# Optimization experiments

Measured on AMD Instinct MI355X. Metric: run time of the kernel, lower is better.

The kernel has to match this reference:

```python
import jax, jax.numpy as jnp
import numpy as np
from jax import lax

B = 8192
C = 16          # conv_channels
H = 256         # hidden_size = W_init.shape[0]
OUT = 10
IN_SIZE = C * 14 * 14  # 3136


def setup_inputs() -> dict:
    key = jax.random.key(0)
    ks = jax.random.split(key, 8)
    x = jax.random.normal(ks[0], (B, 1, 28, 28), dtype=jnp.float32)
    conv_w = jax.random.normal(ks[1], (C, 1, 3, 3), dtype=jnp.float32) * 0.1
    conv_b = jax.random.normal(ks[2], (C,), dtype=jnp.float32) * 0.1
    W_in = jax.random.normal(ks[3], (H, IN_SIZE), dtype=jnp.float32) * 0.02
    b_in = jax.random.normal(ks[4], (H,), dtype=jnp.float32) * 0.02
    W_out = jax.random.normal(ks[5], (OUT, H), dtype=jnp.float32) * 0.05
    b_out = jax.random.normal(ks[6], (OUT,), dtype=jnp.float32) * 0.05
    # register_buffer('W', W_init * 1e-5)
    W = jax.random.normal(ks[7], (H, H), dtype=jnp.float32) * 1e-5
    return {"x": x, "conv_w": conv_w, "conv_b": conv_b, "W_in": W_in,
            "b_in": b_in, "W_out": W_out, "b_out": b_out, "W": W}


def reference(x, conv_w, conv_b, W_in, b_in, W_out, b_out, W):
    # Conv2d(1, C, 3, padding=1) + ReLU
    y = lax.conv_general_dilated(
        x, conv_w, window_strides=(1, 1), padding="SAME",
        dimension_numbers=("NCHW", "OIHW", "NCHW"))
    y = jax.nn.relu(y + conv_b[None, :, None, None])
    # MaxPool2d(2): 28x28 -> 14x14
    y = lax.reduce_window(y, -jnp.inf, lax.max,
                          (1, 1, 2, 2), (1, 1, 2, 2), "VALID")
    conv_flat = y.reshape(y.shape[0], -1)  # [B, C*14*14], NCHW order matches torch view
    # step 0: E_t = Linear(conv_flat); r_t starts at zeros
    E0 = conv_flat @ W_in.T + b_in            # [B, H]
    r = jax.nn.relu(E0)                       # relu(0 @ W + E0 + 0)
    # 9 more steps with zero input -> E_t = b_in
    for _ in range(9):
        r = jax.nn.relu(r @ W + b_in + r)
    return r @ W_out.T + b_out                # [B, 10]
```

## Files before the change

kernel.cpp:

```cpp
#include <hip/hip_runtime.h>

typedef _Float16 f16x8 __attribute__((ext_vector_type(8)));
typedef _Float16 f16x4 __attribute__((ext_vector_type(4)));
typedef float f32x4 __attribute__((ext_vector_type(4)));

__device__ __forceinline__ void gload16(const void* g, void* l) {
  __builtin_amdgcn_global_load_lds(
      (__attribute__((address_space(1))) void*)g,
      (__attribute__((address_space(3))) void*)l, 16, 0, 0);
}

#define W_SCALE 4096.0f
#define W_UNSCALE (1.0f / 4096.0f)

#define SWZA(k, row) (((k) & ~31) | (((k) & 31) ^ (((row) & 3) << 3)))

__global__ __launch_bounds__(256) void conv_pool_kernel(
    const float* __restrict__ x,
    const float* __restrict__ cw,
    const float* __restrict__ cb,
    _Float16* __restrict__ out) {
  __shared__ float wsm[144];
  __shared__ float bsm[16];
  int tid = threadIdx.x;
  if (tid < 144) wsm[tid] = cw[tid];
  if (tid < 16) bsm[tid] = cb[tid];
  __syncthreads();
  if (tid >= 196) return;
  int b = blockIdx.x;
  int ph = tid / 14, pw = tid - ph * 14;
  const float* xb = x + b * 784;
  float xv[4][4];
  int r0 = 2 * ph - 1, c0 = 2 * pw - 1;
#pragma unroll
  for (int i = 0; i < 4; ++i) {
    int r = r0 + i;
#pragma unroll
    for (int j = 0; j < 4; ++j) {
      int c = c0 + j;
      xv[i][j] = (r >= 0 && r < 28 && c >= 0 && c < 28) ? xb[r * 28 + c] : 0.f;
    }
  }
#pragma unroll
  for (int ch = 0; ch < 16; ++ch) {
    float a0 = bsm[ch], a1 = a0, a2 = a0, a3 = a0;
#pragma unroll
    for (int i = 0; i < 3; ++i)
#pragma unroll
      for (int j = 0; j < 3; ++j) {
        float wv = wsm[ch * 9 + i * 3 + j];
        a0 = fmaf(wv, xv[i][j],     a0);
        a1 = fmaf(wv, xv[i][j + 1], a1);
        a2 = fmaf(wv, xv[i + 1][j],     a2);
        a3 = fmaf(wv, xv[i + 1][j + 1], a3);
      }
    float m = fmaxf(fmaxf(a0, a1), fmaxf(a2, a3));
    m = fmaxf(m, 0.f);
    int k = ch * 196 + tid;
    out[b * 3136 + SWZA(k, b)] = (_Float16)m;
  }
}

__global__ __launch_bounds__(256) void win_cvt_kernel(
    const float* __restrict__ in,
    _Float16* __restrict__ out) {
  int n = blockIdx.x, tid = threadIdx.x;
  const float* src = in + (size_t)n * 3136;
  _Float16* dst = out + (size_t)n * 3136;
#pragma unroll
  for (int it = 0; it < 4; ++it) {
    int idx = it * 256 + tid;
    if (idx < 784) {
      int k0 = idx * 4;
      float4 v = *(const float4*)(src + k0);
      f16x4 h = {(_Float16)v.x, (_Float16)v.y, (_Float16)v.z, (_Float16)v.w};
      *(f16x4*)(dst + SWZA(k0, n)) = h;
    }
  }
}

__global__ void wt_cvt_kernel(const float* __restrict__ W,
                              _Float16* __restrict__ Wt) {
  int i = blockIdx.x * 256 + threadIdx.x;
  int k = i >> 8, n = i & 255;
  Wt[n * 256 + k] = (_Float16)(W[k * 256 + n] * W_SCALE);
}

__global__ __launch_bounds__(256) void gemm1_kernel(
    const _Float16* __restrict__ A,
    const _Float16* __restrict__ Bw,
    const float* __restrict__ bias,
    float* __restrict__ Rf,
    _Float16* __restrict__ Rb) {
  const int K = 3136;
  __shared__ __align__(16) _Float16 As[64 * 32];
  __shared__ __align__(16) _Float16 Bs[128 * 32];
  int tid = threadIdx.x, lane = tid & 63, wid = tid >> 6;
  int bm = blockIdx.x * 64, bn = blockIdx.y * 128;
  f32x4 zero = {0.f, 0.f, 0.f, 0.f};
  f32x4 acc[2][4];
#pragma unroll
  for (int i = 0; i < 2; ++i)
#pragma unroll
    for (int j = 0; j < 4; ++j) acc[i][j] = zero;

  const _Float16* Ag  = A  + (size_t)(bm + wid * 16 + (lane >> 2)) * K + (lane & 3) * 8;
  const _Float16* Bg0 = Bw + (size_t)(bn + wid * 32 + (lane >> 2)) * K + (lane & 3) * 8;
  const _Float16* Bg1 = Bg0 + 16 * K;
  _Float16* Asw  = As + wid * 512;
  _Float16* Bsw0 = Bs + wid * 1024;
  _Float16* Bsw1 = Bsw0 + 512;

  int wm = (wid & 1) * 32, wn = (wid >> 1) * 64;
  int koff = (lane >> 4) * 8;
  for (int k0 = 0; k0 < K; k0 += 32) {
    __syncthreads();
    gload16(Ag + k0, Asw);
    gload16(Bg0 + k0, Bsw0);
    gload16(Bg1 + k0, Bsw1);
    __syncthreads();
    f16x8 af[2];
#pragma unroll
    for (int mi = 0; mi < 2; ++mi) {
      int ar = wm + mi * 16 + (lane & 15);
      af[mi] = *(const f16x8*)(As + ar * 32 + (koff ^ ((ar & 3) << 3)));
    }
#pragma unroll
    for (int ni = 0; ni < 4; ++ni) {
      int br = wn + ni * 16 + (lane & 15);
      f16x8 bf = *(const f16x8*)(Bs + br * 32 + (koff ^ ((br & 3) << 3)));
      acc[0][ni] = __builtin_amdgcn_mfma_f32_16x16x32_f16(af[0], bf, acc[0][ni], 0, 0, 0);
      acc[1][ni] = __builtin_amdgcn_mfma_f32_16x16x32_f16(af[1], bf, acc[1][ni], 0, 0, 0);
    }
  }
  int rg = (lane >> 4) * 4, cl = lane & 15;
#pragma unroll
  for (int mi = 0; mi < 2; ++mi)
#pragma unroll
    for (int ni = 0; ni < 4; ++ni)
#pragma unroll
      for (int j = 0; j < 4; ++j) {
        int m = bm + wm + mi * 16 + rg + j;
        int n = bn + wn + ni * 16 + cl;
        float v = fmaxf(acc[mi][ni][j] + bias[n], 0.f);
        Rf[m * 256 + n] = v;
        Rb[m * 256 + n] = (_Float16)v;
      }
}

__global__ __launch_bounds__(512, 2) void rnn_persist_kernel(
    const _Float16* __restrict__ Rb,
    const float*    __restrict__ Rf,
    const _Float16* __restrict__ Wt,
    const float*    __restrict__ b_in,
    const float*    __restrict__ Wo,
    const float*    __restrict__ bo,
    float*          __restrict__ out)
{
  __shared__ __align__(16) _Float16 r_lds[32 * 256];
  int tid = threadIdx.x, lane = tid & 63, wid = tid >> 6;
  int wr = wid >> 2, wc = wid & 3;
  int bm = blockIdx.x * 32;

  f16x8 wfr[8][4];
#pragma unroll
  for (int kk = 0; kk < 8; ++kk)
#pragma unroll
    for (int ni = 0; ni < 4; ++ni) {
      int n = wc * 64 + ni * 16 + (lane & 15);
      int kpos = kk * 32 + (lane >> 4) * 8;
      wfr[kk][ni] = *(const f16x8*)(Wt + n * 256 + kpos);
    }

  float breg[4];
  float rres[4][4];
  int rrow = wr * 16 + (lane >> 4) * 4;
#pragma unroll
  for (int ni = 0; ni < 4; ++ni) {
    int col = wc * 64 + ni * 16 + (lane & 15);
    breg[ni] = b_in[col];
#pragma unroll
    for (int j = 0; j < 4; ++j)
      rres[ni][j] = Rf[(size_t)(bm + rrow + j) * 256 + col];
  }

#pragma unroll
  for (int it = 0; it < 2; ++it) {
    int idx = it * 512 + tid;
    int row = idx >> 5;
    int kc = (idx & 31) * 8;
    f16x8 v = *(const f16x8*)(Rb + (size_t)(bm + row) * 256 + kc);
    *(f16x8*)(r_lds + row * 256 + (kc ^ ((row & 7) << 3))) = v;
  }

  int arow = wr * 16 + (lane & 15);
  int aswz = (arow & 7) << 3;
  for (int s = 0; s < 9; ++s) {
    __syncthreads();
    f32x4 acc[4];
#pragma unroll
    for (int ni = 0; ni < 4; ++ni) acc[ni] = (f32x4){0.f, 0.f, 0.f, 0.f};
#pragma unroll
    for (int kk = 0; kk < 8; ++kk) {
      int kpos = kk * 32 + (lane >> 4) * 8;
      f16x8 af = *(const f16x8*)(r_lds + arow * 256 + (kpos ^ aswz));
#pragma unroll
      for (int ni = 0; ni < 4; ++ni)
        acc[ni] = __builtin_amdgcn_mfma_f32_16x16x32_f16(af, wfr[kk][ni], acc[ni], 0, 0, 0);
    }
    __syncthreads();
#pragma unroll
    for (int ni = 0; ni < 4; ++ni) {
      int col = wc * 64 + ni * 16 + (lane & 15);
#pragma unroll
      for (int j = 0; j < 4; ++j) {
        float v = fmaxf(fmaf(acc[ni][j], W_UNSCALE, breg[ni] + rres[ni][j]), 0.f);
        rres[ni][j] = v;
        int row = rrow + j;
        r_lds[row * 256 + (col ^ ((row & 7) << 3))] = (_Float16)v;
      }
    }
  }
  __syncthreads();

  if (tid < 320) {
    int row = tid / 10, o = tid - row * 10;
    int rswz = (row & 7) << 3;
    float accd = 0.f;
    for (int kc = 0; kc < 256; kc += 8) {
      f16x8 rv = *(const f16x8*)(r_lds + row * 256 + (kc ^ rswz));
      const float* wp = Wo + o * 256 + kc;
#pragma unroll
      for (int j = 0; j < 8; ++j) accd = fmaf((float)rv[j], wp[j], accd);
    }
    out[(size_t)(bm + row) * 10 + o] = accd + bo[o];
  }
}

extern "C" void kernel_launch(void* const* d_in, const int* in_sizes, int n_in,
                              void* d_out, int out_size, void* d_ws, size_t ws_size,
                              hipStream_t stream) {
  const float* x      = (const float*)d_in[0];
  const float* conv_w = (const float*)d_in[1];
  const float* conv_b = (const float*)d_in[2];
  const float* W_in   = (const float*)d_in[3];
  const float* b_in   = (const float*)d_in[4];
  const float* W_out  = (const float*)d_in[5];
  const float* b_out  = (const float*)d_in[6];
  const float* W      = (const float*)d_in[7];
  float* out = (float*)d_out;

  char* ws = (char*)d_ws;
  size_t o = 0;
  _Float16* conv_flat = (_Float16*)(ws + o); o += (size_t)8192 * 3136 * 2;
  _Float16* W_in_h    = (_Float16*)(ws + o); o += (size_t)256 * 3136 * 2;
  _Float16* Wt_h      = (_Float16*)(ws + o); o += (size_t)256 * 256 * 2;
  float*    Rf0       = (float*)(ws + o);    o += (size_t)8192 * 256 * 4;
  _Float16* Rb0       = (_Float16*)(ws + o); o += (size_t)8192 * 256 * 2;

  win_cvt_kernel<<<256, 256, 0, stream>>>(W_in, W_in_h);
  wt_cvt_kernel<<<256, 256, 0, stream>>>(W, Wt_h);
  conv_pool_kernel<<<8192, 256, 0, stream>>>(x, conv_w, conv_b, conv_flat);
  gemm1_kernel<<<dim3(128, 2), 256, 0, stream>>>(conv_flat, W_in_h, b_in, Rf0, Rb0);
  rnn_persist_kernel<<<256, 512, 0, stream>>>(Rb0, Rf0, Wt_h, b_in, W_out, b_out, out);
}
```

Before: 188.3 us.

## Split-K gemm1 with atomics, interleaved tile layout, packed fp16 conv

Splits the 3136-long K of the first GEMM across 7 z-blocks that accumulate into a bias-initialised fp32 buffer with atomic adds. This raises the grid from 256 to 1792 blocks so the whole GPU is occupied, and the ReLU moves into the RNN kernel's load. Conv output and W_in are stored in a 16-row, 32-k tiled layout so each wave's global-to-LDS load is one contiguous chunk. The conv now uses packed half2 FMAs, and the separate fp16 copy of R is dropped. In exchange it adds atomic traffic, an extra init kernel, and computes the conv in reduced fp16 precision.

```diff
diff --git a/kernel.cpp b/kernel.cpp
--- a/kernel.cpp
+++ b/kernel.cpp
@@ -2,6 +2,7 @@
 
 typedef _Float16 f16x8 __attribute__((ext_vector_type(8)));
 typedef _Float16 f16x4 __attribute__((ext_vector_type(4)));
+typedef _Float16 h2   __attribute__((ext_vector_type(2)));
 typedef float f32x4 __attribute__((ext_vector_type(4)));
 
 __device__ __forceinline__ void gload16(const void* g, void* l) {
@@ -13,18 +14,19 @@
 #define W_SCALE 4096.0f
 #define W_UNSCALE (1.0f / 4096.0f)
 
-#define SWZA(k, row) (((k) & ~31) | (((k) & 31) ^ (((row) & 3) << 3)))
+#define ISL(row, k) (((row) >> 4) * 50176 + ((k) >> 5) * 512 + \
+                     ((((k) >> 3) & 3) << 7) + (((row) & 15) << 3) + ((k) & 7))
 
 __global__ __launch_bounds__(256) void conv_pool_kernel(
     const float* __restrict__ x,
     const float* __restrict__ cw,
     const float* __restrict__ cb,
     _Float16* __restrict__ out) {
-  __shared__ float wsm[144];
-  __shared__ float bsm[16];
+  __shared__ h2 wsm[144];
+  __shared__ h2 bsm[16];
   int tid = threadIdx.x;
-  if (tid < 144) wsm[tid] = cw[tid];
-  if (tid < 16) bsm[tid] = cb[tid];
+  if (tid < 144) { float w = cw[tid]; wsm[tid] = h2{(_Float16)w, (_Float16)w}; }
+  if (tid < 16)  { float b = cb[tid]; bsm[tid] = h2{(_Float16)b, (_Float16)b}; }
   __syncthreads();
   if (tid >= 196) return;
   int b = blockIdx.x;
@@ -41,23 +43,30 @@
       xv[i][j] = (r >= 0 && r < 28 && c >= 0 && c < 28) ? xb[r * 28 + c] : 0.f;
     }
   }
+  h2 xp[4][3];
+#pragma unroll
+  for (int i = 0; i < 4; ++i)
+#pragma unroll
+    for (int j = 0; j < 3; ++j)
+      xp[i][j] = h2{(_Float16)xv[i][j], (_Float16)xv[i][j + 1]};
+
+  int outbase = (b >> 4) * 50176 + ((b & 15) << 3);
 #pragma unroll
   for (int ch = 0; ch < 16; ++ch) {
-    float a0 = bsm[ch], a1 = a0, a2 = a0, a3 = a0;
+    h2 a01 = bsm[ch], a23 = bsm[ch];
 #pragma unroll
     for (int i = 0; i < 3; ++i)
 #pragma unroll
       for (int j = 0; j < 3; ++j) {
-        float wv = wsm[ch * 9 + i * 3 + j];
-        a0 = fmaf(wv, xv[i][j],     a0);
-        a1 = fmaf(wv, xv[i][j + 1], a1);
-        a2 = fmaf(wv, xv[i + 1][j],     a2);
-        a3 = fmaf(wv, xv[i + 1][j + 1], a3);
+        h2 wv = wsm[ch * 9 + i * 3 + j];
+        a01 = __builtin_elementwise_fma(wv, xp[i][j], a01);
+        a23 = __builtin_elementwise_fma(wv, xp[i + 1][j], a23);
       }
-    float m = fmaxf(fmaxf(a0, a1), fmaxf(a2, a3));
-    m = fmaxf(m, 0.f);
+    h2 m2 = __builtin_elementwise_max(a01, a23);
+    _Float16 m = m2[0] > m2[1] ? m2[0] : m2[1];
+    m = m > (_Float16)0.f ? m : (_Float16)0.f;
     int k = ch * 196 + tid;
-    out[b * 3136 + SWZA(k, b)] = (_Float16)m;
+    out[outbase + ((k >> 5) << 9) + ((((k) >> 3) & 3) << 7) + (k & 7)] = m;
   }
 }
 
@@ -66,7 +75,6 @@
     _Float16* __restrict__ out) {
   int n = blockIdx.x, tid = threadIdx.x;
   const float* src = in + (size_t)n * 3136;
-  _Float16* dst = out + (size_t)n * 3136;
 #pragma unroll
   for (int it = 0; it < 4; ++it) {
     int idx = it * 256 + tid;
@@ -74,7 +82,7 @@
       int k0 = idx * 4;
       float4 v = *(const float4*)(src + k0);
       f16x4 h = {(_Float16)v.x, (_Float16)v.y, (_Float16)v.z, (_Float16)v.w};
-      *(f16x4*)(dst + SWZA(k0, n)) = h;
+      *(f16x4*)(out + ISL(n, k0)) = h;
     }
   }
 }
@@ -86,53 +94,56 @@
   Wt[n * 256 + k] = (_Float16)(W[k * 256 + n] * W_SCALE);
 }
 
+__global__ void init_rf_kernel(const float* __restrict__ b_in,
+                               float* __restrict__ Rf) {
+  int idx = blockIdx.x * 256 + threadIdx.x;
+  float4 b4 = ((const float4*)b_in)[idx & 63];
+  ((float4*)Rf)[idx] = b4;
+}
+
 __global__ __launch_bounds__(256) void gemm1_kernel(
     const _Float16* __restrict__ A,
     const _Float16* __restrict__ Bw,
-    const float* __restrict__ bias,
-    float* __restrict__ Rf,
-    _Float16* __restrict__ Rb) {
-  const int K = 3136;
-  __shared__ __align__(16) _Float16 As[64 * 32];
-  __shared__ __align__(16) _Float16 Bs[128 * 32];
+    float* __restrict__ Rf) {
+  __shared__ __align__(16) _Float16 As[2048];
+  __shared__ __align__(16) _Float16 Bs[4096];
   int tid = threadIdx.x, lane = tid & 63, wid = tid >> 6;
   int bm = blockIdx.x * 64, bn = blockIdx.y * 128;
-  f32x4 zero = {0.f, 0.f, 0.f, 0.f};
   f32x4 acc[2][4];
 #pragma unroll
   for (int i = 0; i < 2; ++i)
 #pragma unroll
-    for (int j = 0; j < 4; ++j) acc[i][j] = zero;
-
-  const _Float16* Ag  = A  + (size_t)(bm + wid * 16 + (lane >> 2)) * K + (lane & 3) * 8;
-  const _Float16* Bg0 = Bw + (size_t)(bn + wid * 32 + (lane >> 2)) * K + (lane & 3) * 8;
-  const _Float16* Bg1 = Bg0 + 16 * K;
+    for (int j = 0; j < 4; ++j) acc[i][j] = (f32x4){0.f, 0.f, 0.f, 0.f};
+
+  const _Float16* Ag  = A  + ((bm >> 4) + wid) * 50176 + lane * 8;
+  const _Float16* Bg0 = Bw + ((bn >> 4) + 2 * wid) * 50176 + lane * 8;
+  const _Float16* Bg1 = Bg0 + 50176;
   _Float16* Asw  = As + wid * 512;
-  _Float16* Bsw0 = Bs + wid * 1024;
+  _Float16* Bsw0 = Bs + 2 * wid * 512;
   _Float16* Bsw1 = Bsw0 + 512;
 
-  int wm = (wid & 1) * 32, wn = (wid >> 1) * 64;
-  int koff = (lane >> 4) * 8;
-  for (int k0 = 0; k0 < K; k0 += 32) {
-    __syncthreads();
-    gload16(Ag + k0, Asw);
-    gload16(Bg0 + k0, Bsw0);
-    gload16(Bg1 + k0, Bsw1);
+  int c0 = blockIdx.z * 14;
+  int rko = ((lane >> 4) << 7) + ((lane & 15) << 3);
+  int ga = (wid & 1) * 2, gb = (wid >> 1) * 4;
+  for (int t = 0; t < 14; ++t) {
+    int coff = (c0 + t) * 512;
+    __syncthreads();
+    gload16(Ag + coff, Asw);
+    gload16(Bg0 + coff, Bsw0);
+    gload16(Bg1 + coff, Bsw1);
     __syncthreads();
     f16x8 af[2];
 #pragma unroll
-    for (int mi = 0; mi < 2; ++mi) {
-      int ar = wm + mi * 16 + (lane & 15);
-      af[mi] = *(const f16x8*)(As + ar * 32 + (koff ^ ((ar & 3) << 3)));
-    }
+    for (int mi = 0; mi < 2; ++mi)
+      af[mi] = *(const f16x8*)(As + (ga + mi) * 512 + rko);
 #pragma unroll
     for (int ni = 0; ni < 4; ++ni) {
-      int br = wn + ni * 16 + (lane & 15);
-      f16x8 bf = *(const f16x8*)(Bs + br * 32 + (koff ^ ((br & 3) << 3)));
+      f16x8 bf = *(const f16x8*)(Bs + (gb + ni) * 512 + rko);
       acc[0][ni] = __builtin_amdgcn_mfma_f32_16x16x32_f16(af[0], bf, acc[0][ni], 0, 0, 0);
       acc[1][ni] = __builtin_amdgcn_mfma_f32_16x16x32_f16(af[1], bf, acc[1][ni], 0, 0, 0);
     }
   }
+  int wm = (wid & 1) * 32, wn = (wid >> 1) * 64;
   int rg = (lane >> 4) * 4, cl = lane & 15;
 #pragma unroll
   for (int mi = 0; mi < 2; ++mi)
@@ -142,14 +153,12 @@
       for (int j = 0; j < 4; ++j) {
         int m = bm + wm + mi * 16 + rg + j;
         int n = bn + wn + ni * 16 + cl;
-        float v = fmaxf(acc[mi][ni][j] + bias[n], 0.f);
-        Rf[m * 256 + n] = v;
-        Rb[m * 256 + n] = (_Float16)v;
+        __hip_atomic_fetch_add(&Rf[m * 256 + n], acc[mi][ni][j],
+                               __ATOMIC_RELAXED, __HIP_MEMORY_SCOPE_AGENT);
       }
 }
 
 __global__ __launch_bounds__(512, 2) void rnn_persist_kernel(
-    const _Float16* __restrict__ Rb,
     const float*    __restrict__ Rf,
     const _Float16* __restrict__ Wt,
     const float*    __restrict__ b_in,
@@ -181,7 +190,7 @@
     breg[ni] = b_in[col];
 #pragma unroll
     for (int j = 0; j < 4; ++j)
-      rres[ni][j] = Rf[(size_t)(bm + rrow + j) * 256 + col];
+      rres[ni][j] = fmaxf(Rf[(size_t)(bm + rrow + j) * 256 + col], 0.f);
   }
 
 #pragma unroll
@@ -189,8 +198,15 @@
     int idx = it * 512 + tid;
     int row = idx >> 5;
     int kc = (idx & 31) * 8;
-    f16x8 v = *(const f16x8*)(Rb + (size_t)(bm + row) * 256 + kc);
-    *(f16x8*)(r_lds + row * 256 + (kc ^ ((row & 7) << 3))) = v;
+    const float* src = Rf + (size_t)(bm + row) * 256 + kc;
+    f32x4 v0 = *(const f32x4*)src;
+    f32x4 v1 = *(const f32x4*)(src + 4);
+    f16x8 h;
+#pragma unroll
+    for (int j = 0; j < 4; ++j) h[j] = (_Float16)fmaxf(v0[j], 0.f);
+#pragma unroll
+    for (int j = 0; j < 4; ++j) h[4 + j] = (_Float16)fmaxf(v1[j], 0.f);
+    *(f16x8*)(r_lds + row * 256 + (kc ^ ((row & 7) << 3))) = h;
   }
 
   int arow = wr * 16 + (lane & 15);
@@ -256,11 +272,11 @@
   _Float16* W_in_h    = (_Float16*)(ws + o); o += (size_t)256 * 3136 * 2;
   _Float16* Wt_h      = (_Float16*)(ws + o); o += (size_t)256 * 256 * 2;
   float*    Rf0       = (float*)(ws + o);    o += (size_t)8192 * 256 * 4;
-  _Float16* Rb0       = (_Float16*)(ws + o); o += (size_t)8192 * 256 * 2;
 
   win_cvt_kernel<<<256, 256, 0, stream>>>(W_in, W_in_h);
   wt_cvt_kernel<<<256, 256, 0, stream>>>(W, Wt_h);
+  init_rf_kernel<<<2048, 256, 0, stream>>>(b_in, Rf0);
   conv_pool_kernel<<<8192, 256, 0, stream>>>(x, conv_w, conv_b, conv_flat);
-  gemm1_kernel<<<dim3(128, 2), 256, 0, stream>>>(conv_flat, W_in_h, b_in, Rf0, Rb0);
-  rnn_persist_kernel<<<256, 512, 0, stream>>>(Rb0, Rf0, Wt_h, b_in, W_out, b_out, out);
-}
+  gemm1_kernel<<<dim3(128, 2, 7), 256, 0, stream>>>(conv_flat, W_in_h, Rf0);
+  rnn_persist_kernel<<<256, 512, 0, stream>>>(Rf0, Wt_h, b_in, W_out, b_out, out);
+}
```

New measurement: 225.8 us. 1.2x slower.
